# Kernel optimization log

Measured on AMD Instinct MI355X. Metric: run time of the kernel, lower is better.

## Reference

```python
import jax, jax.numpy as jnp
import numpy as np

N, L, D, W = 64, 514, 768, 256   # batch, padded token len (incl CLS/SEP), bert dim, max words
H1, H2 = 500, 300                # linear1 out, out_size
LN_EPS = 1e-5


def setup_inputs() -> dict:
    key = jax.random.key(0)
    ks = jax.random.split(key, 6)
    texts = jax.random.normal(ks[0], (N, L, D), dtype=jnp.float32)
    # contiguous ragged spans: lengths in {1,2}, cumulative ends <= 512 = L-2 always
    lens = jax.random.randint(ks[1], (N, W), 1, 3)
    word_ends = jnp.cumsum(lens, axis=1).astype(jnp.int32)
    word_starts = (word_ends - lens).astype(jnp.int32)
    word_length = jax.random.randint(ks[2], (N,), W // 2, W + 1).astype(jnp.int32)
    W1 = jax.random.normal(ks[3], (D, H1), dtype=jnp.float32) * np.float32(1.0 / np.sqrt(D))
    b1 = jnp.zeros((H1,), jnp.float32)
    W2 = jax.random.normal(ks[4], (H1, H2), dtype=jnp.float32) * np.float32(1.0 / np.sqrt(H1))
    b2 = jnp.zeros((H2,), jnp.float32)
    gamma = jnp.ones((H2,), jnp.float32)
    beta = jnp.zeros((H2,), jnp.float32)
    return dict(texts=texts, word_starts=word_starts, word_ends=word_ends,
                word_length=word_length, W1=W1, b1=b1, W2=W2, b2=b2,
                gamma=gamma, beta=beta)


def reference(texts, word_starts, word_ends, word_length, W1, b1, W2, b2, gamma, beta):
    # texts: (N, L, D) BERT output; drop [CLS]/[SEP]
    tok = texts[:, 1:-1, :]  # (N, L-2, D)
    # offset-based segment mean: prefix sums over token axis
    csum = jnp.concatenate([jnp.zeros_like(tok[:, :1]), jnp.cumsum(tok, axis=1)], axis=1)  # (N, L-1, D)
    e = word_ends[:, :, None].astype(jnp.int32)
    s = word_starts[:, :, None].astype(jnp.int32)
    seg_sum = jnp.take_along_axis(csum, e, axis=1) - jnp.take_along_axis(csum, s, axis=1)  # (N, W, D)
    cnt = (word_ends - word_starts).astype(texts.dtype)[:, :, None]
    pooled = seg_sum / jnp.maximum(cnt, 1.0)
    # pad_sequence semantics: words beyond word_length[i] are zero
    mask = (jnp.arange(W)[None, :] < word_length[:, None])[:, :, None]
    pooled = jnp.where(mask, pooled, jnp.zeros((), texts.dtype))
    # MLP + LayerNorm: norm(relu(linear2(relu(linear1(x)))))
    h = jax.nn.relu(pooled @ W1 + b1)
    h = jax.nn.relu(h @ W2 + b2)
    mu = jnp.mean(h, axis=-1, keepdims=True)
    var = jnp.mean(jnp.square(h - mu), axis=-1, keepdims=True)
    return (h - mu) * jax.lax.rsqrt(var + LN_EPS) * gamma + beta  # (N, W, 300)
```

## Files before the change

### kernel.cpp

```cpp
#include <hip/hip_runtime.h>
#include <hip/hip_bf16.h>


#define N_  64
#define L_  514
#define D_  768
#define W_  256
#define H1_ 500
#define H1P 512
#define H2_ 300
#define H2P 320
#define LN_EPS 1e-5f
#define M_  (N_ * W_)

typedef __bf16 bf16x8 __attribute__((ext_vector_type(8)));
typedef float  f32x4  __attribute__((ext_vector_type(4)));

__device__ __forceinline__ void load_lds16(const void* g, void* l) {
    __builtin_amdgcn_global_load_lds(
        (const __attribute__((address_space(1))) void*)g,
        (__attribute__((address_space(3))) void*)l, 16, 0, 0);
}

#define CONV1_ELEMS (H1P * D_)
#define CONV2_ELEMS (H2P * H1P)
#define CONV1_B ((CONV1_ELEMS + 191) / 192)
#define CONV2_B ((CONV2_ELEMS + 191) / 192)

__global__ __launch_bounds__(192) void prep_kernel(
    const float* __restrict__ texts, const int* __restrict__ wstart,
    const int* __restrict__ wend, const int* __restrict__ wlen,
    const float* __restrict__ W1, const float* __restrict__ W2,
    __hip_bfloat16* __restrict__ pooled, __hip_bfloat16* __restrict__ W1T,
    __hip_bfloat16* __restrict__ W2T)
{
    int b = blockIdx.x;
    if (b < M_) {
        int n = b >> 8;
        int w = b & (W_ - 1);
        int s = wstart[b], e = wend[b];
        bool live = (w < wlen[n]);
        int d = threadIdx.x * 4;
        float4 acc = make_float4(0.f, 0.f, 0.f, 0.f);
        if (live) {
            const float* base = texts + ((size_t)n * L_ + 1) * D_ + d;
            for (int i = s; i < e; ++i) {
                float4 v = *reinterpret_cast<const float4*>(base + (size_t)i * D_);
                acc.x += v.x; acc.y += v.y; acc.z += v.z; acc.w += v.w;
            }
            float inv = 1.0f / (float)max(e - s, 1);
            acc.x *= inv; acc.y *= inv; acc.z *= inv; acc.w *= inv;
        }
        union { __hip_bfloat16 h[4]; uint2 u; } o;
        o.h[0] = __float2bfloat16(acc.x); o.h[1] = __float2bfloat16(acc.y);
        o.h[2] = __float2bfloat16(acc.z); o.h[3] = __float2bfloat16(acc.w);
        *reinterpret_cast<uint2*>(pooled + (size_t)b * D_ + d) = o.u;
    } else if (b < M_ + CONV1_B) {
        int t = (b - M_) * 192 + threadIdx.x;
        if (t < CONV1_ELEMS) {
            int n = t / D_, k = t - n * D_;
            float v = (n < H1_) ? W1[(size_t)k * H1_ + n] : 0.f;
            W1T[t] = __float2bfloat16(v);
        }
    } else {
        int t = (b - M_ - CONV1_B) * 192 + threadIdx.x;
        if (t < CONV2_ELEMS) {
            int n = t >> 9, k = t & (H1P - 1);
            float v = (n < H2_ && k < H1_) ? W2[(size_t)k * H2_ + n] : 0.f;
            W2T[t] = __float2bfloat16(v);
        }
    }
}

__global__ __launch_bounds__(512, 1) void gemm1_kernel(
    const ushort* __restrict__ A, const ushort* __restrict__ B,
    const float* __restrict__ b1, ushort* __restrict__ h1)
{
    constexpr int BUFB = 24576;
    __shared__ __align__(16) char bufs[4 * BUFB];
    const int tid  = threadIdx.x;
    const int wave = tid >> 6, lane = tid & 63;
    const int wm = wave >> 1, wn = wave & 1;
    const int t256 = (blockIdx.x & 7) * 32 + (blockIdx.x >> 3);
    const int bm = (t256 >> 2) * 256, bn = (t256 & 3) * 128;
    const int lrow = lane >> 2, lslot = lane & 3;
    const int g = lane >> 4, fr = lane & 15;

    f32x4 acc[4][4] = {};

    auto stage = [&](int buf, int kt) {
        char* base = bufs + buf * BUFB;
        #pragma unroll
        for (int c0 = 0; c0 < 3; ++c0) {
            int c = wave + c0 * 8;
            int row; const ushort* src;
            if (c < 16) { row = c * 16 + lrow; src = A + (size_t)(bm + row) * D_; }
            else        { row = (c - 16) * 16 + lrow; src = B + (size_t)(bn + row) * D_; }
            int sslot = lslot ^ ((row >> 1) & 3);
            load_lds16(src + kt + sslot * 8, base + c * 1024);
        }
    };

    auto compute = [&](int t) {
        const char* base = bufs + (t & 3) * BUFB;
        bf16x8 af[4], bf[4];
        #pragma unroll
        for (int mi = 0; mi < 4; ++mi) {
            int r = wm * 64 + mi * 16 + fr;
            af[mi] = *(const bf16x8*)(base + r * 64 + ((g ^ ((r >> 1) & 3)) << 4));
        }
        #pragma unroll
        for (int ni = 0; ni < 4; ++ni) {
            int r = wn * 64 + ni * 16 + fr;
            bf[ni] = *(const bf16x8*)(base + 16384 + r * 64 + ((g ^ ((r >> 1) & 3)) << 4));
        }
        __builtin_amdgcn_s_setprio(1);
        #pragma unroll
        for (int mi = 0; mi < 4; ++mi)
            #pragma unroll
            for (int ni = 0; ni < 4; ++ni)
                acc[mi][ni] = __builtin_amdgcn_mfma_f32_16x16x32_bf16(
                    af[mi], bf[ni], acc[mi][ni], 0, 0, 0);
        __builtin_amdgcn_s_setprio(0);
    };

    stage(0, 0); stage(1, 32); stage(2, 64);
    for (int t = 0; t < 22; ++t) {
        asm volatile("s_waitcnt vmcnt(6)" ::: "memory");
        __builtin_amdgcn_s_barrier();
        if (t + 3 < 24) stage((t + 3) & 3, (t + 3) * 32);
        compute(t);
    }
    asm volatile("s_waitcnt vmcnt(3)" ::: "memory");
    __builtin_amdgcn_s_barrier();
    compute(22);
    asm volatile("s_waitcnt vmcnt(0)" ::: "memory");
    __builtin_amdgcn_s_barrier();
    compute(23);

    #pragma unroll
    for (int mi = 0; mi < 4; ++mi)
        #pragma unroll
        for (int ni = 0; ni < 4; ++ni) {
            int col = bn + wn * 64 + ni * 16 + fr;
            float bv = (col < H1_) ? b1[col] : 0.f;
            #pragma unroll
            for (int j = 0; j < 4; ++j) {
                int row = bm + wm * 64 + mi * 16 + g * 4 + j;
                float v = acc[mi][ni][j] + bv;
                ((__hip_bfloat16*)h1)[(size_t)row * H1P + col] =
                    __float2bfloat16(v > 0.f ? v : 0.f);
            }
        }
}

__global__ __launch_bounds__(512, 1) void gemm2_ln_kernel(
    const ushort* __restrict__ A, const ushort* __restrict__ B,
    const float* __restrict__ b2, const float* __restrict__ gamma,
    const float* __restrict__ beta, float* __restrict__ out)
{
    constexpr int BUFB = 24576;
    __shared__ __align__(16) char bufs[4 * BUFB];
    __shared__ float red[2][32][4][2];
    const int tid  = threadIdx.x;
    const int wave = tid >> 6, lane = tid & 63;
    const int wm = wave >> 2, wn = wave & 3;
    const int bm = blockIdx.x * 64;
    const int lrow = lane >> 2, lslot = lane & 3;
    const int g = lane >> 4, fr = lane & 15;

    f32x4 acc[2][5] = {};

    auto stage = [&](int buf, int kt) {
        char* base = bufs + buf * BUFB;
        #pragma unroll
        for (int c0 = 0; c0 < 3; ++c0) {
            int c = wave + c0 * 8;
            int row; const ushort* src;
            if (c < 4) { row = c * 16 + lrow; src = A + (size_t)(bm + row) * H1P; }
            else       { row = (c - 4) * 16 + lrow; src = B + (size_t)row * H1P; }
            int sslot = lslot ^ ((row >> 1) & 3);
            load_lds16(src + kt + sslot * 8, base + c * 1024);
        }
    };

    auto compute = [&](int t) {
        const char* base = bufs + (t & 3) * BUFB;
        bf16x8 af[2], bf[5];
        #pragma unroll
        for (int mi = 0; mi < 2; ++mi) {
            int r = wm * 32 + mi * 16 + fr;
            af[mi] = *(const bf16x8*)(base + r * 64 + ((g ^ ((r >> 1) & 3)) << 4));
        }
        #pragma unroll
        for (int ni = 0; ni < 5; ++ni) {
            int r = wn * 80 + ni * 16 + fr;
            bf[ni] = *(const bf16x8*)(base + 4096 + r * 64 + ((g ^ ((r >> 1) & 3)) << 4));
        }
        __builtin_amdgcn_s_setprio(1);
        #pragma unroll
        for (int mi = 0; mi < 2; ++mi)
            #pragma unroll
            for (int ni = 0; ni < 5; ++ni)
                acc[mi][ni] = __builtin_amdgcn_mfma_f32_16x16x32_bf16(
                    af[mi], bf[ni], acc[mi][ni], 0, 0, 0);
        __builtin_amdgcn_s_setprio(0);
    };

    stage(0, 0); stage(1, 32); stage(2, 64);
    for (int t = 0; t < 14; ++t) {
        asm volatile("s_waitcnt vmcnt(6)" ::: "memory");
        __builtin_amdgcn_s_barrier();
        if (t + 3 < 16) stage((t + 3) & 3, (t + 3) * 32);
        compute(t);
    }
    asm volatile("s_waitcnt vmcnt(3)" ::: "memory");
    __builtin_amdgcn_s_barrier();
    compute(14);
    asm volatile("s_waitcnt vmcnt(0)" ::: "memory");
    __builtin_amdgcn_s_barrier();
    compute(15);

    float vals[2][5][4];
    float rsum[2][4] = {}, rsq[2][4] = {};
    #pragma unroll
    for (int ni = 0; ni < 5; ++ni) {
        int col = wn * 80 + ni * 16 + fr;
        float bv = (col < H2_) ? b2[col] : 0.f;
        #pragma unroll
        for (int mi = 0; mi < 2; ++mi)
            #pragma unroll
            for (int j = 0; j < 4; ++j) {
                float v = acc[mi][ni][j] + bv;
                v = v > 0.f ? v : 0.f;
                vals[mi][ni][j] = v;
                rsum[mi][j] += v;
                rsq[mi][j]  += v * v;
            }
    }
    #pragma unroll
    for (int off = 1; off < 16; off <<= 1)
        #pragma unroll
        for (int mi = 0; mi < 2; ++mi)
            #pragma unroll
            for (int j = 0; j < 4; ++j) {
                rsum[mi][j] += __shfl_xor(rsum[mi][j], off);
                rsq[mi][j]  += __shfl_xor(rsq[mi][j], off);
            }
    if (fr == 0) {
        #pragma unroll
        for (int mi = 0; mi < 2; ++mi)
            #pragma unroll
            for (int j = 0; j < 4; ++j) {
                int r32 = mi * 16 + g * 4 + j;
                red[wm][r32][wn][0] = rsum[mi][j];
                red[wm][r32][wn][1] = rsq[mi][j];
            }
    }
    __syncthreads();
    #pragma unroll
    for (int mi = 0; mi < 2; ++mi) {
        #pragma unroll
        for (int j = 0; j < 4; ++j) {
            int r32 = mi * 16 + g * 4 + j;
            float S  = red[wm][r32][0][0] + red[wm][r32][1][0]
                     + red[wm][r32][2][0] + red[wm][r32][3][0];
            float SQ = red[wm][r32][0][1] + red[wm][r32][1][1]
                     + red[wm][r32][2][1] + red[wm][r32][3][1];
            float mu   = S * (1.0f / H2_);
            float var  = SQ * (1.0f / H2_) - mu * mu;
            float rstd = rsqrtf(var + LN_EPS);
            int row = bm + wm * 32 + r32;
            #pragma unroll
            for (int ni = 0; ni < 5; ++ni) {
                int col = wn * 80 + ni * 16 + fr;
                if (col < H2_)
                    out[(size_t)row * H2_ + col] =
                        (vals[mi][ni][j] - mu) * rstd * gamma[col] + beta[col];
            }
        }
    }
}

extern "C" void kernel_launch(void* const* d_in, const int* in_sizes, int n_in,
                              void* d_out, int out_size, void* d_ws, size_t ws_size,
                              hipStream_t stream)
{
    const float* texts  = (const float*)d_in[0];
    const int*   wstart = (const int*)  d_in[1];
    const int*   wend   = (const int*)  d_in[2];
    const int*   wlen   = (const int*)  d_in[3];
    const float* W1     = (const float*)d_in[4];
    const float* b1     = (const float*)d_in[5];
    const float* W2     = (const float*)d_in[6];
    const float* b2     = (const float*)d_in[7];
    const float* gamma  = (const float*)d_in[8];
    const float* beta   = (const float*)d_in[9];
    float* out = (float*)d_out;

    ushort* pooled = (ushort*)d_ws;
    ushort* h1     = pooled + (size_t)M_ * D_;
    ushort* W1T    = h1 + (size_t)M_ * H1P;
    ushort* W2T    = W1T + (size_t)H1P * D_;

    prep_kernel<<<M_ + CONV1_B + CONV2_B, 192, 0, stream>>>(
        texts, wstart, wend, wlen, W1, W2,
        (__hip_bfloat16*)pooled, (__hip_bfloat16*)W1T, (__hip_bfloat16*)W2T);

    gemm1_kernel<<<256, 512, 0, stream>>>(pooled, W1T, b1, h1);

    gemm2_ln_kernel<<<M_ / 64, 512, 0, stream>>>(h1, W2T, b2, gamma, beta, out);
}
```

Measured before the change: 57.10 us.

## Load GEMM B-operand fragments directly into registers, bypassing LDS staging

In both GEMM kernels, the weight (B) tiles are no longer staged through LDS. Each wave now loads its B fragments straight from global memory into registers, prefetched one k-step ahead with a double-buffered register pair. Only the A tile still goes through the LDS ring, which shrinks the LDS buffers and cuts LDS read/write traffic. The trade-offs are duplicated global/L2 reads of B across waves and more live VGPRs. The hand-tuned vmcnt waits now mix register and LDS loads, and in the tail iterations the pending count may no longer guarantee that the last A stage has landed before the barrier.

```diff
diff --git a/kernel.cpp b/kernel.cpp
--- a/kernel.cpp
+++ b/kernel.cpp
@@ -76,7 +76,7 @@
     const ushort* __restrict__ A, const ushort* __restrict__ B,
     const float* __restrict__ b1, ushort* __restrict__ h1)
 {
-    constexpr int BUFB = 24576;
+    constexpr int BUFB = 16384;
     __shared__ __align__(16) char bufs[4 * BUFB];
     const int tid  = threadIdx.x;
     const int wave = tid >> 6, lane = tid & 63;
@@ -88,55 +88,56 @@
 
     f32x4 acc[4][4] = {};
 
-    auto stage = [&](int buf, int kt) {
+    auto stageA = [&](int buf, int kt) {
         char* base = bufs + buf * BUFB;
         #pragma unroll
-        for (int c0 = 0; c0 < 3; ++c0) {
+        for (int c0 = 0; c0 < 2; ++c0) {
             int c = wave + c0 * 8;
-            int row; const ushort* src;
-            if (c < 16) { row = c * 16 + lrow; src = A + (size_t)(bm + row) * D_; }
-            else        { row = (c - 16) * 16 + lrow; src = B + (size_t)(bn + row) * D_; }
+            int row = c * 16 + lrow;
             int sslot = lslot ^ ((row >> 1) & 3);
-            load_lds16(src + kt + sslot * 8, base + c * 1024);
-        }
-    };
-
-    auto compute = [&](int t) {
+            load_lds16(A + (size_t)(bm + row) * D_ + kt + sslot * 8,
+                       base + c * 1024);
+        }
+    };
+    const ushort* Bw = B + (size_t)(bn + wn * 64 + fr) * D_ + g * 8;
+    auto loadB = [&](bf16x8* dst, int kt) {
+        #pragma unroll
+        for (int ni = 0; ni < 4; ++ni)
+            dst[ni] = *(const bf16x8*)(Bw + (size_t)(ni * 16) * D_ + kt);
+    };
+
+    auto compute = [&](int t, const bf16x8* bcur) {
         const char* base = bufs + (t & 3) * BUFB;
-        bf16x8 af[4], bf[4];
+        bf16x8 af[4];
         #pragma unroll
         for (int mi = 0; mi < 4; ++mi) {
             int r = wm * 64 + mi * 16 + fr;
             af[mi] = *(const bf16x8*)(base + r * 64 + ((g ^ ((r >> 1) & 3)) << 4));
         }
-        #pragma unroll
-        for (int ni = 0; ni < 4; ++ni) {
-            int r = wn * 64 + ni * 16 + fr;
-            bf[ni] = *(const bf16x8*)(base + 16384 + r * 64 + ((g ^ ((r >> 1) & 3)) << 4));
-        }
         __builtin_amdgcn_s_setprio(1);
         #pragma unroll
         for (int mi = 0; mi < 4; ++mi)
             #pragma unroll
             for (int ni = 0; ni < 4; ++ni)
                 acc[mi][ni] = __builtin_amdgcn_mfma_f32_16x16x32_bf16(
-                    af[mi], bf[ni], acc[mi][ni], 0, 0, 0);
+                    af[mi], bcur[ni], acc[mi][ni], 0, 0, 0);
         __builtin_amdgcn_s_setprio(0);
     };
 
-    stage(0, 0); stage(1, 32); stage(2, 64);
-    for (int t = 0; t < 22; ++t) {
-        asm volatile("s_waitcnt vmcnt(6)" ::: "memory");
+    bf16x8 bcur[4], bnext[4];
+    stageA(0, 0); stageA(1, 32); stageA(2, 64);
+    loadB(bcur, 0);
+
+    constexpr int NT = 24;
+    for (int t = 0; t < NT; ++t) {
+        asm volatile("s_waitcnt vmcnt(8)" ::: "memory");
         __builtin_amdgcn_s_barrier();
-        if (t + 3 < 24) stage((t + 3) & 3, (t + 3) * 32);
-        compute(t);
-    }
-    asm volatile("s_waitcnt vmcnt(3)" ::: "memory");
-    __builtin_amdgcn_s_barrier();
-    compute(22);
-    asm volatile("s_waitcnt vmcnt(0)" ::: "memory");
-    __builtin_amdgcn_s_barrier();
-    compute(23);
+        if (t + 1 < NT) loadB(bnext, (t + 1) * 32);
+        if (t + 3 < NT) stageA((t + 3) & 3, (t + 3) * 32);
+        compute(t, bcur);
+        #pragma unroll
+        for (int ni = 0; ni < 4; ++ni) bcur[ni] = bnext[ni];
+    }
 
     #pragma unroll
     for (int mi = 0; mi < 4; ++mi)
@@ -159,7 +160,7 @@
     const float* __restrict__ b2, const float* __restrict__ gamma,
     const float* __restrict__ beta, float* __restrict__ out)
 {
-    constexpr int BUFB = 24576;
+    constexpr int BUFB = 4096;
     __shared__ __align__(16) char bufs[4 * BUFB];
     __shared__ float red[2][32][4][2];
     const int tid  = threadIdx.x;
@@ -171,55 +172,53 @@
 
     f32x4 acc[2][5] = {};
 
-    auto stage = [&](int buf, int kt) {
-        char* base = bufs + buf * BUFB;
-        #pragma unroll
-        for (int c0 = 0; c0 < 3; ++c0) {
-            int c = wave + c0 * 8;
-            int row; const ushort* src;
-            if (c < 4) { row = c * 16 + lrow; src = A + (size_t)(bm + row) * H1P; }
-            else       { row = (c - 4) * 16 + lrow; src = B + (size_t)row * H1P; }
+    auto stageA = [&](int buf, int kt) {
+        if (wave < 4) {
+            int row = wave * 16 + lrow;
             int sslot = lslot ^ ((row >> 1) & 3);
-            load_lds16(src + kt + sslot * 8, base + c * 1024);
-        }
-    };
-
-    auto compute = [&](int t) {
+            load_lds16(A + (size_t)(bm + row) * H1P + kt + sslot * 8,
+                       bufs + buf * BUFB + wave * 1024);
+        }
+    };
+    const ushort* Bw = B + (size_t)(wn * 80 + fr) * H1P + g * 8;
+    auto loadB = [&](bf16x8* dst, int kt) {
+        #pragma unroll
+        for (int ni = 0; ni < 5; ++ni)
+            dst[ni] = *(const bf16x8*)(Bw + (size_t)(ni * 16) * H1P + kt);
+    };
+
+    auto compute = [&](int t, const bf16x8* bcur) {
         const char* base = bufs + (t & 3) * BUFB;
-        bf16x8 af[2], bf[5];
+        bf16x8 af[2];
         #pragma unroll
         for (int mi = 0; mi < 2; ++mi) {
             int r = wm * 32 + mi * 16 + fr;
             af[mi] = *(const bf16x8*)(base + r * 64 + ((g ^ ((r >> 1) & 3)) << 4));
         }
-        #pragma unroll
-        for (int ni = 0; ni < 5; ++ni) {
-            int r = wn * 80 + ni * 16 + fr;
-            bf[ni] = *(const bf16x8*)(base + 4096 + r * 64 + ((g ^ ((r >> 1) & 3)) << 4));
-        }
         __builtin_amdgcn_s_setprio(1);
         #pragma unroll
         for (int mi = 0; mi < 2; ++mi)
             #pragma unroll
             for (int ni = 0; ni < 5; ++ni)
                 acc[mi][ni] = __builtin_amdgcn_mfma_f32_16x16x32_bf16(
-                    af[mi], bf[ni], acc[mi][ni], 0, 0, 0);
+                    af[mi], bcur[ni], acc[mi][ni], 0, 0, 0);
         __builtin_amdgcn_s_setprio(0);
     };
 
-    stage(0, 0); stage(1, 32); stage(2, 64);
-    for (int t = 0; t < 14; ++t) {
-        asm volatile("s_waitcnt vmcnt(6)" ::: "memory");
+    bf16x8 bcur[5], bnext[5];
+    stageA(0, 0); stageA(1, 32); stageA(2, 64);
+    loadB(bcur, 0);
+
+    constexpr int NT = 16;
+    for (int t = 0; t < NT; ++t) {
+        asm volatile("s_waitcnt vmcnt(7)" ::: "memory");
         __builtin_amdgcn_s_barrier();
-        if (t + 3 < 16) stage((t + 3) & 3, (t + 3) * 32);
-        compute(t);
-    }
-    asm volatile("s_waitcnt vmcnt(3)" ::: "memory");
-    __builtin_amdgcn_s_barrier();
-    compute(14);
-    asm volatile("s_waitcnt vmcnt(0)" ::: "memory");
-    __builtin_amdgcn_s_barrier();
-    compute(15);
+        if (t + 1 < NT) loadB(bnext, (t + 1) * 32);
+        if (t + 3 < NT) stageA((t + 3) & 3, (t + 3) * 32);
+        compute(t, bcur);
+        #pragma unroll
+        for (int ni = 0; ni < 5; ++ni) bcur[ni] = bnext[ni];
+    }
 
     float vals[2][5][4];
     float rsum[2][4] = {}, rsq[2][4] = {};
```

New measurement: 90.33 us. 58.2% more time.

## Fuse segment-mean pooling into GEMM1 A-tile loads, drop pooled buffer

Applied to the files above, without the earlier changes.

Segment-mean pooling moves out of the prep kernel and into GEMM1's A operand staging. Each thread loads fp32 token rows for its word, averages them, converts to bf16 and writes the result into swizzled LDS. This removes the pooled bf16 intermediate's write and re-read, leaving only a small weight-conversion kernel. In exchange the pipeline drops from a 4-stage async global-to-LDS prefetch to a 2-stage register-prefetch loop with full barriers. Each of the 4 column blocks per row block now re-reads the fp32 texts rows, so more raw bytes are fetched and latency hiding may be weaker.

```diff
diff --git a/kernel.cpp b/kernel.cpp
--- a/kernel.cpp
+++ b/kernel.cpp
@@ -24,95 +24,109 @@
 
 #define CONV1_ELEMS (H1P * D_)
 #define CONV2_ELEMS (H2P * H1P)
-#define CONV1_B ((CONV1_ELEMS + 191) / 192)
-#define CONV2_B ((CONV2_ELEMS + 191) / 192)
-
-__global__ __launch_bounds__(192) void prep_kernel(
+#define CONV1_B (CONV1_ELEMS / 256)
+#define CONV2_B (CONV2_ELEMS / 256)
+
+__global__ __launch_bounds__(256) void conv_kernel(
+    const float* __restrict__ W1, const float* __restrict__ W2,
+    __hip_bfloat16* __restrict__ W1T, __hip_bfloat16* __restrict__ W2T)
+{
+    int b = blockIdx.x;
+    if (b < CONV1_B) {
+        int t = b * 256 + threadIdx.x;
+        int n = t / D_, k = t - n * D_;
+        float v = (n < H1_) ? W1[(size_t)k * H1_ + n] : 0.f;
+        W1T[t] = __float2bfloat16(v);
+    } else {
+        int t = (b - CONV1_B) * 256 + threadIdx.x;
+        int n = t >> 9, k = t & (H1P - 1);
+        float v = (n < H2_ && k < H1_) ? W2[(size_t)k * H2_ + n] : 0.f;
+        W2T[t] = __float2bfloat16(v);
+    }
+}
+
+__global__ __launch_bounds__(512, 1) void gemm1_kernel(
     const float* __restrict__ texts, const int* __restrict__ wstart,
     const int* __restrict__ wend, const int* __restrict__ wlen,
-    const float* __restrict__ W1, const float* __restrict__ W2,
-    __hip_bfloat16* __restrict__ pooled, __hip_bfloat16* __restrict__ W1T,
-    __hip_bfloat16* __restrict__ W2T)
+    const ushort* __restrict__ B, const float* __restrict__ b1,
+    ushort* __restrict__ h1)
 {
-    int b = blockIdx.x;
-    if (b < M_) {
-        int n = b >> 8;
-        int w = b & (W_ - 1);
-        int s = wstart[b], e = wend[b];
-        bool live = (w < wlen[n]);
-        int d = threadIdx.x * 4;
-        float4 acc = make_float4(0.f, 0.f, 0.f, 0.f);
-        if (live) {
-            const float* base = texts + ((size_t)n * L_ + 1) * D_ + d;
-            for (int i = s; i < e; ++i) {
-                float4 v = *reinterpret_cast<const float4*>(base + (size_t)i * D_);
-                acc.x += v.x; acc.y += v.y; acc.z += v.z; acc.w += v.w;
-            }
-            float inv = 1.0f / (float)max(e - s, 1);
-            acc.x *= inv; acc.y *= inv; acc.z *= inv; acc.w *= inv;
-        }
-        union { __hip_bfloat16 h[4]; uint2 u; } o;
-        o.h[0] = __float2bfloat16(acc.x); o.h[1] = __float2bfloat16(acc.y);
-        o.h[2] = __float2bfloat16(acc.z); o.h[3] = __float2bfloat16(acc.w);
-        *reinterpret_cast<uint2*>(pooled + (size_t)b * D_ + d) = o.u;
-    } else if (b < M_ + CONV1_B) {
-        int t = (b - M_) * 192 + threadIdx.x;
-        if (t < CONV1_ELEMS) {
-            int n = t / D_, k = t - n * D_;
-            float v = (n < H1_) ? W1[(size_t)k * H1_ + n] : 0.f;
-            W1T[t] = __float2bfloat16(v);
-        }
-    } else {
-        int t = (b - M_ - CONV1_B) * 192 + threadIdx.x;
-        if (t < CONV2_ELEMS) {
-            int n = t >> 9, k = t & (H1P - 1);
-            float v = (n < H2_ && k < H1_) ? W2[(size_t)k * H2_ + n] : 0.f;
-            W2T[t] = __float2bfloat16(v);
-        }
-    }
-}
-
-__global__ __launch_bounds__(512, 1) void gemm1_kernel(
-    const ushort* __restrict__ A, const ushort* __restrict__ B,
-    const float* __restrict__ b1, ushort* __restrict__ h1)
-{
-    constexpr int BUFB = 24576;
-    __shared__ __align__(16) char bufs[4 * BUFB];
+    __shared__ __align__(16) char Abuf[2][16384];
+    __shared__ __align__(16) char Bbuf[2][8192];
+
     const int tid  = threadIdx.x;
     const int wave = tid >> 6, lane = tid & 63;
     const int wm = wave >> 1, wn = wave & 1;
     const int t256 = (blockIdx.x & 7) * 32 + (blockIdx.x >> 3);
-    const int bm = (t256 >> 2) * 256, bn = (t256 & 3) * 128;
+    const int n  = t256 >> 2;
+    const int bm = n * 256, bn = (t256 & 3) * 128;
     const int lrow = lane >> 2, lslot = lane & 3;
     const int g = lane >> 4, fr = lane & 15;
 
+    const int prow  = tid >> 1;
+    const int phalf = tid & 1;
+    const int s = wstart[bm + prow];
+    const int e = wend[bm + prow];
+    const bool live = (prow < wlen[n]);
+    const bool two  = live && (e - s > 1);
+    const float inv = live ? 1.0f / (float)max(e - s, 1) : 0.f;
+    const float* trow = texts + ((size_t)n * L_ + 1 + s) * D_ + phalf * 16;
+
     f32x4 acc[4][4] = {};
 
-    auto stage = [&](int buf, int kt) {
-        char* base = bufs + buf * BUFB;
-        #pragma unroll
-        for (int c0 = 0; c0 < 3; ++c0) {
-            int c = wave + c0 * 8;
-            int row; const ushort* src;
-            if (c < 16) { row = c * 16 + lrow; src = A + (size_t)(bm + row) * D_; }
-            else        { row = (c - 16) * 16 + lrow; src = B + (size_t)(bn + row) * D_; }
-            int sslot = lslot ^ ((row >> 1) & 3);
-            load_lds16(src + kt + sslot * 8, base + c * 1024);
-        }
-    };
-
+    auto issueA = [&](float4* pf, int kt) {
+        if (live) {
+            const float4* p0 = (const float4*)(trow + kt);
+            pf[0] = p0[0]; pf[1] = p0[1]; pf[2] = p0[2]; pf[3] = p0[3];
+        }
+        if (two) {
+            const float4* p1 = (const float4*)(trow + kt + D_);
+            pf[4] = p1[0]; pf[5] = p1[1]; pf[6] = p1[2]; pf[7] = p1[3];
+        }
+    };
+    auto writeA = [&](const float4* pf, int buf) {
+        union { __hip_bfloat16 h[8]; uint4 u; } o0, o1;
+        #pragma unroll
+        for (int j = 0; j < 4; ++j) {
+            float4 a = pf[j], b2v = pf[4 + j];
+            float x0 = two ? a.x + b2v.x : a.x;
+            float x1 = two ? a.y + b2v.y : a.y;
+            float x2 = two ? a.z + b2v.z : a.z;
+            float x3 = two ? a.w + b2v.w : a.w;
+            x0 = live ? x0 * inv : 0.f;  x1 = live ? x1 * inv : 0.f;
+            x2 = live ? x2 * inv : 0.f;  x3 = live ? x3 * inv : 0.f;
+            if (j < 2) {
+                o0.h[j*4+0] = __float2bfloat16(x0); o0.h[j*4+1] = __float2bfloat16(x1);
+                o0.h[j*4+2] = __float2bfloat16(x2); o0.h[j*4+3] = __float2bfloat16(x3);
+            } else {
+                o1.h[(j-2)*4+0] = __float2bfloat16(x0); o1.h[(j-2)*4+1] = __float2bfloat16(x1);
+                o1.h[(j-2)*4+2] = __float2bfloat16(x2); o1.h[(j-2)*4+3] = __float2bfloat16(x3);
+            }
+        }
+        const int swz = (prow >> 1) & 3;
+        char* base = Abuf[buf] + prow * 64;
+        *(uint4*)(base + (((phalf*2 + 0) ^ swz) << 4)) = o0.u;
+        *(uint4*)(base + (((phalf*2 + 1) ^ swz) << 4)) = o1.u;
+    };
+    auto stageB = [&](int buf, int kt) {
+        int row = wave * 16 + lrow;
+        int sslot = lslot ^ ((row >> 1) & 3);
+        load_lds16(B + (size_t)(bn + row) * D_ + kt + sslot * 8,
+                   Bbuf[buf] + wave * 1024);
+    };
     auto compute = [&](int t) {
-        const char* base = bufs + (t & 3) * BUFB;
+        const char* ab = Abuf[t & 1];
+        const char* bb = Bbuf[t & 1];
         bf16x8 af[4], bf[4];
         #pragma unroll
         for (int mi = 0; mi < 4; ++mi) {
             int r = wm * 64 + mi * 16 + fr;
-            af[mi] = *(const bf16x8*)(base + r * 64 + ((g ^ ((r >> 1) & 3)) << 4));
+            af[mi] = *(const bf16x8*)(ab + r * 64 + ((g ^ ((r >> 1) & 3)) << 4));
         }
         #pragma unroll
         for (int ni = 0; ni < 4; ++ni) {
             int r = wn * 64 + ni * 16 + fr;
-            bf[ni] = *(const bf16x8*)(base + 16384 + r * 64 + ((g ^ ((r >> 1) & 3)) << 4));
+            bf[ni] = *(const bf16x8*)(bb + r * 64 + ((g ^ ((r >> 1) & 3)) << 4));
         }
         __builtin_amdgcn_s_setprio(1);
         #pragma unroll
@@ -124,19 +138,22 @@
         __builtin_amdgcn_s_setprio(0);
     };
 
-    stage(0, 0); stage(1, 32); stage(2, 64);
-    for (int t = 0; t < 22; ++t) {
-        asm volatile("s_waitcnt vmcnt(6)" ::: "memory");
-        __builtin_amdgcn_s_barrier();
-        if (t + 3 < 24) stage((t + 3) & 3, (t + 3) * 32);
+    float4 pf[8];
+    issueA(pf, 0);
+    stageB(0, 0);
+    writeA(pf, 0);
+    __syncthreads();
+
+    constexpr int NT = 24;
+    for (int t = 0; t < NT; ++t) {
+        if (t + 1 < NT) {
+            issueA(pf, (t + 1) * 32);
+            stageB((t + 1) & 1, (t + 1) * 32);
+        }
         compute(t);
-    }
-    asm volatile("s_waitcnt vmcnt(3)" ::: "memory");
-    __builtin_amdgcn_s_barrier();
-    compute(22);
-    asm volatile("s_waitcnt vmcnt(0)" ::: "memory");
-    __builtin_amdgcn_s_barrier();
-    compute(23);
+        if (t + 1 < NT) writeA(pf, (t + 1) & 1);
+        __syncthreads();
+    }
 
     #pragma unroll
     for (int mi = 0; mi < 4; ++mi)
@@ -298,16 +315,15 @@
     const float* beta   = (const float*)d_in[9];
     float* out = (float*)d_out;
 
-    ushort* pooled = (ushort*)d_ws;
-    ushort* h1     = pooled + (size_t)M_ * D_;
-    ushort* W1T    = h1 + (size_t)M_ * H1P;
-    ushort* W2T    = W1T + (size_t)H1P * D_;
-
-    prep_kernel<<<M_ + CONV1_B + CONV2_B, 192, 0, stream>>>(
-        texts, wstart, wend, wlen, W1, W2,
-        (__hip_bfloat16*)pooled, (__hip_bfloat16*)W1T, (__hip_bfloat16*)W2T);
-
-    gemm1_kernel<<<256, 512, 0, stream>>>(pooled, W1T, b1, h1);
+    ushort* h1  = (ushort*)d_ws;
+    ushort* W1T = h1 + (size_t)M_ * H1P;
+    ushort* W2T = W1T + (size_t)H1P * D_;
+
+    conv_kernel<<<CONV1_B + CONV2_B, 256, 0, stream>>>(
+        W1, W2, (__hip_bfloat16*)W1T, (__hip_bfloat16*)W2T);
+
+    gemm1_kernel<<<256, 512, 0, stream>>>(
+        texts, wstart, wend, wlen, W1T, b1, h1);
 
     gemm2_ln_kernel<<<M_ / 64, 512, 0, stream>>>(h1, W2T, b2, gamma, beta, out);
 }
```

Result: slower. 71.56 us (+25.3%).

## Fuse prep, GEMM1 and GEMM2+LayerNorm into one cooperative persistent kernel

Applied to the files above, without the earlier changes.

Replaces the three launches (pooling plus weight transposes, GEMM1, GEMM2 with LayerNorm) with a single cooperative kernel of 256 blocks, using grid-wide syncs between the phases. Pooling is redone per block so that each wave handles 8 words with 3 float4 loads per lane. The goal is to remove launch gaps and per-kernel ramp-up and tail time. In exchange the kernel pays for grid.sync, and the pooling phase now runs on only 256 blocks instead of about 16K small blocks, which may reduce memory-level parallelism for the pooling reads.

```diff
diff --git a/kernel.cpp b/kernel.cpp
--- a/kernel.cpp
+++ b/kernel.cpp
@@ -1,6 +1,9 @@
 #include <hip/hip_runtime.h>
 #include <hip/hip_bf16.h>
-
+#include <hip/hip_cooperative_groups.h>
+
+
+namespace cg = cooperative_groups;
 
 #define N_  64
 #define L_  514
@@ -12,6 +15,8 @@
 #define H2P 320
 #define LN_EPS 1e-5f
 #define M_  (N_ * W_)
+#define CONV1_ELEMS (H1P * D_)
+#define CONV2_ELEMS (H2P * H1P)
 
 typedef __bf16 bf16x8 __attribute__((ext_vector_type(8)));
 typedef float  f32x4  __attribute__((ext_vector_type(4)));
@@ -22,261 +27,252 @@
         (__attribute__((address_space(3))) void*)l, 16, 0, 0);
 }
 
-#define CONV1_ELEMS (H1P * D_)
-#define CONV2_ELEMS (H2P * H1P)
-#define CONV1_B ((CONV1_ELEMS + 191) / 192)
-#define CONV2_B ((CONV2_ELEMS + 191) / 192)
-
-__global__ __launch_bounds__(192) void prep_kernel(
+__device__ __forceinline__ uint2 pack4(f32x4 v) {
+    union { __hip_bfloat16 h[4]; uint2 u; } o;
+    o.h[0] = __float2bfloat16(v[0]); o.h[1] = __float2bfloat16(v[1]);
+    o.h[2] = __float2bfloat16(v[2]); o.h[3] = __float2bfloat16(v[3]);
+    return o.u;
+}
+
+__global__ __launch_bounds__(512, 1) void fused_kernel(
     const float* __restrict__ texts, const int* __restrict__ wstart,
     const int* __restrict__ wend, const int* __restrict__ wlen,
     const float* __restrict__ W1, const float* __restrict__ W2,
-    __hip_bfloat16* __restrict__ pooled, __hip_bfloat16* __restrict__ W1T,
-    __hip_bfloat16* __restrict__ W2T)
+    const float* __restrict__ b1, const float* __restrict__ b2,
+    const float* __restrict__ gamma, const float* __restrict__ beta,
+    ushort* __restrict__ pooled, ushort* __restrict__ h1,
+    ushort* __restrict__ W1T, ushort* __restrict__ W2T,
+    float* __restrict__ out)
 {
-    int b = blockIdx.x;
-    if (b < M_) {
-        int n = b >> 8;
-        int w = b & (W_ - 1);
-        int s = wstart[b], e = wend[b];
-        bool live = (w < wlen[n]);
-        int d = threadIdx.x * 4;
-        float4 acc = make_float4(0.f, 0.f, 0.f, 0.f);
-        if (live) {
-            const float* base = texts + ((size_t)n * L_ + 1) * D_ + d;
-            for (int i = s; i < e; ++i) {
-                float4 v = *reinterpret_cast<const float4*>(base + (size_t)i * D_);
-                acc.x += v.x; acc.y += v.y; acc.z += v.z; acc.w += v.w;
-            }
-            float inv = 1.0f / (float)max(e - s, 1);
-            acc.x *= inv; acc.y *= inv; acc.z *= inv; acc.w *= inv;
-        }
-        union { __hip_bfloat16 h[4]; uint2 u; } o;
-        o.h[0] = __float2bfloat16(acc.x); o.h[1] = __float2bfloat16(acc.y);
-        o.h[2] = __float2bfloat16(acc.z); o.h[3] = __float2bfloat16(acc.w);
-        *reinterpret_cast<uint2*>(pooled + (size_t)b * D_ + d) = o.u;
-    } else if (b < M_ + CONV1_B) {
-        int t = (b - M_) * 192 + threadIdx.x;
-        if (t < CONV1_ELEMS) {
-            int n = t / D_, k = t - n * D_;
-            float v = (n < H1_) ? W1[(size_t)k * H1_ + n] : 0.f;
-            W1T[t] = __float2bfloat16(v);
-        }
-    } else {
-        int t = (b - M_ - CONV1_B) * 192 + threadIdx.x;
-        if (t < CONV2_ELEMS) {
-            int n = t >> 9, k = t & (H1P - 1);
-            float v = (n < H2_ && k < H1_) ? W2[(size_t)k * H2_ + n] : 0.f;
-            W2T[t] = __float2bfloat16(v);
-        }
-    }
-}
-
-__global__ __launch_bounds__(512, 1) void gemm1_kernel(
-    const ushort* __restrict__ A, const ushort* __restrict__ B,
-    const float* __restrict__ b1, ushort* __restrict__ h1)
-{
-    constexpr int BUFB = 24576;
-    __shared__ __align__(16) char bufs[4 * BUFB];
-    const int tid  = threadIdx.x;
+    __shared__ __align__(16) char bufs[4 * 24576];
+    __shared__ float red[2][32][4][2];
+
+    const int b = blockIdx.x;
+    const int tid = threadIdx.x;
     const int wave = tid >> 6, lane = tid & 63;
-    const int wm = wave >> 1, wn = wave & 1;
-    const int t256 = (blockIdx.x & 7) * 32 + (blockIdx.x >> 3);
-    const int bm = (t256 >> 2) * 256, bn = (t256 & 3) * 128;
+    const int swz = (b & 7) * 32 + (b >> 3);
     const int lrow = lane >> 2, lslot = lane & 3;
     const int g = lane >> 4, fr = lane & 15;
 
-    f32x4 acc[4][4] = {};
-
-    auto stage = [&](int buf, int kt) {
-        char* base = bufs + buf * BUFB;
-        #pragma unroll
-        for (int c0 = 0; c0 < 3; ++c0) {
-            int c = wave + c0 * 8;
-            int row; const ushort* src;
-            if (c < 16) { row = c * 16 + lrow; src = A + (size_t)(bm + row) * D_; }
-            else        { row = (c - 16) * 16 + lrow; src = B + (size_t)(bn + row) * D_; }
-            int sslot = lslot ^ ((row >> 1) & 3);
-            load_lds16(src + kt + sslot * 8, base + c * 1024);
-        }
-    };
-
-    auto compute = [&](int t) {
-        const char* base = bufs + (t & 3) * BUFB;
-        bf16x8 af[4], bf[4];
-        #pragma unroll
-        for (int mi = 0; mi < 4; ++mi) {
-            int r = wm * 64 + mi * 16 + fr;
-            af[mi] = *(const bf16x8*)(base + r * 64 + ((g ^ ((r >> 1) & 3)) << 4));
-        }
-        #pragma unroll
-        for (int ni = 0; ni < 4; ++ni) {
-            int r = wn * 64 + ni * 16 + fr;
-            bf[ni] = *(const bf16x8*)(base + 16384 + r * 64 + ((g ^ ((r >> 1) & 3)) << 4));
-        }
-        __builtin_amdgcn_s_setprio(1);
+    {
+        for (int t = b * 512 + tid; t < CONV1_ELEMS; t += 256 * 512) {
+            int nn = t / D_, k = t - nn * D_;
+            float v = (nn < H1_) ? W1[(size_t)k * H1_ + nn] : 0.f;
+            ((__hip_bfloat16*)W1T)[t] = __float2bfloat16(v);
+        }
+        for (int t = b * 512 + tid; t < CONV2_ELEMS; t += 256 * 512) {
+            int nn = t >> 9, k = t & (H1P - 1);
+            float v = (nn < H2_ && k < H1_) ? W2[(size_t)k * H2_ + nn] : 0.f;
+            ((__hip_bfloat16*)W2T)[t] = __float2bfloat16(v);
+        }
+        const int n = swz >> 2, q = swz & 3;
+        for (int i = 0; i < 8; ++i) {
+            int wl  = q * 64 + wave * 8 + i;
+            int idx = n * W_ + wl;
+            int s = wstart[idx], e = wend[idx];
+            bool live = wl < wlen[n];
+            float inv = 1.0f / (float)max(e - s, 1);
+            f32x4 a0 = {}, a1 = {}, a2 = {};
+            if (live) {
+                const float* base = texts + ((size_t)n * L_ + 1 + s) * D_ + lane * 4;
+                for (int r = 0; r < e - s; ++r) {
+                    const float* p = base + (size_t)r * D_;
+                    a0 += *(const f32x4*)(p);
+                    a1 += *(const f32x4*)(p + 256);
+                    a2 += *(const f32x4*)(p + 512);
+                }
+                a0 *= inv; a1 *= inv; a2 *= inv;
+            }
+            __hip_bfloat16* dst = (__hip_bfloat16*)pooled + (size_t)idx * D_ + lane * 4;
+            *(uint2*)(dst)       = pack4(a0);
+            *(uint2*)(dst + 256) = pack4(a1);
+            *(uint2*)(dst + 512) = pack4(a2);
+        }
+    }
+    cg::this_grid().sync();
+
+    {
+        const int wm = wave >> 1, wn = wave & 1;
+        const int bm = (swz >> 2) * 256, bn = (swz & 3) * 128;
+        f32x4 acc[4][4] = {};
+
+        auto stage = [&](int buf, int kt) {
+            char* base = bufs + buf * 24576;
+            #pragma unroll
+            for (int c0 = 0; c0 < 3; ++c0) {
+                int c = wave + c0 * 8;
+                int row; const ushort* src;
+                if (c < 16) { row = c * 16 + lrow;        src = pooled + (size_t)(bm + row) * D_; }
+                else        { row = (c - 16) * 16 + lrow; src = W1T + (size_t)(bn + row) * D_; }
+                int sslot = lslot ^ ((row >> 1) & 3);
+                load_lds16(src + kt + sslot * 8, base + c * 1024);
+            }
+        };
+        auto compute = [&](int t) {
+            const char* base = bufs + (t & 3) * 24576;
+            bf16x8 af[4], bf[4];
+            #pragma unroll
+            for (int mi = 0; mi < 4; ++mi) {
+                int r = wm * 64 + mi * 16 + fr;
+                af[mi] = *(const bf16x8*)(base + r * 64 + ((g ^ ((r >> 1) & 3)) << 4));
+            }
+            #pragma unroll
+            for (int ni = 0; ni < 4; ++ni) {
+                int r = wn * 64 + ni * 16 + fr;
+                bf[ni] = *(const bf16x8*)(base + 16384 + r * 64 + ((g ^ ((r >> 1) & 3)) << 4));
+            }
+            __builtin_amdgcn_s_setprio(1);
+            #pragma unroll
+            for (int mi = 0; mi < 4; ++mi)
+                #pragma unroll
+                for (int ni = 0; ni < 4; ++ni)
+                    acc[mi][ni] = __builtin_amdgcn_mfma_f32_16x16x32_bf16(
+                        af[mi], bf[ni], acc[mi][ni], 0, 0, 0);
+            __builtin_amdgcn_s_setprio(0);
+        };
+
+        stage(0, 0); stage(1, 32); stage(2, 64);
+        for (int t = 0; t < 22; ++t) {
+            asm volatile("s_waitcnt vmcnt(6)" ::: "memory");
+            __builtin_amdgcn_s_barrier();
+            if (t + 3 < 24) stage((t + 3) & 3, (t + 3) * 32);
+            compute(t);
+        }
+        asm volatile("s_waitcnt vmcnt(3)" ::: "memory");
+        __builtin_amdgcn_s_barrier();
+        compute(22);
+        asm volatile("s_waitcnt vmcnt(0)" ::: "memory");
+        __builtin_amdgcn_s_barrier();
+        compute(23);
+
         #pragma unroll
         for (int mi = 0; mi < 4; ++mi)
             #pragma unroll
-            for (int ni = 0; ni < 4; ++ni)
-                acc[mi][ni] = __builtin_amdgcn_mfma_f32_16x16x32_bf16(
-                    af[mi], bf[ni], acc[mi][ni], 0, 0, 0);
-        __builtin_amdgcn_s_setprio(0);
-    };
-
-    stage(0, 0); stage(1, 32); stage(2, 64);
-    for (int t = 0; t < 22; ++t) {
-        asm volatile("s_waitcnt vmcnt(6)" ::: "memory");
+            for (int ni = 0; ni < 4; ++ni) {
+                int col = bn + wn * 64 + ni * 16 + fr;
+                float bv = (col < H1_) ? b1[col] : 0.f;
+                #pragma unroll
+                for (int j = 0; j < 4; ++j) {
+                    int row = bm + wm * 64 + mi * 16 + g * 4 + j;
+                    float v = acc[mi][ni][j] + bv;
+                    ((__hip_bfloat16*)h1)[(size_t)row * H1P + col] =
+                        __float2bfloat16(v > 0.f ? v : 0.f);
+                }
+            }
+    }
+    cg::this_grid().sync();
+
+    {
+        const int wm = wave >> 2, wn = wave & 3;
+        const int bm = swz * 64;
+        f32x4 acc[2][5] = {};
+
+        auto stage = [&](int buf, int kt) {
+            char* base = bufs + buf * 24576;
+            #pragma unroll
+            for (int c0 = 0; c0 < 3; ++c0) {
+                int c = wave + c0 * 8;
+                int row; const ushort* src;
+                if (c < 4) { row = c * 16 + lrow;       src = h1 + (size_t)(bm + row) * H1P; }
+                else       { row = (c - 4) * 16 + lrow; src = W2T + (size_t)row * H1P; }
+                int sslot = lslot ^ ((row >> 1) & 3);
+                load_lds16(src + kt + sslot * 8, base + c * 1024);
+            }
+        };
+        auto compute = [&](int t) {
+            const char* base = bufs + (t & 3) * 24576;
+            bf16x8 af[2], bf[5];
+            #pragma unroll
+            for (int mi = 0; mi < 2; ++mi) {
+                int r = wm * 32 + mi * 16 + fr;
+                af[mi] = *(const bf16x8*)(base + r * 64 + ((g ^ ((r >> 1) & 3)) << 4));
+            }
+            #pragma unroll
+            for (int ni = 0; ni < 5; ++ni) {
+                int r = wn * 80 + ni * 16 + fr;
+                bf[ni] = *(const bf16x8*)(base + 4096 + r * 64 + ((g ^ ((r >> 1) & 3)) << 4));
+            }
+            __builtin_amdgcn_s_setprio(1);
+            #pragma unroll
+            for (int mi = 0; mi < 2; ++mi)
+                #pragma unroll
+                for (int ni = 0; ni < 5; ++ni)
+                    acc[mi][ni] = __builtin_amdgcn_mfma_f32_16x16x32_bf16(
+                        af[mi], bf[ni], acc[mi][ni], 0, 0, 0);
+            __builtin_amdgcn_s_setprio(0);
+        };
+
+        stage(0, 0); stage(1, 32); stage(2, 64);
+        for (int t = 0; t < 14; ++t) {
+            asm volatile("s_waitcnt vmcnt(6)" ::: "memory");
+            __builtin_amdgcn_s_barrier();
+            if (t + 3 < 16) stage((t + 3) & 3, (t + 3) * 32);
+            compute(t);
+        }
+        asm volatile("s_waitcnt vmcnt(3)" ::: "memory");
         __builtin_amdgcn_s_barrier();
-        if (t + 3 < 24) stage((t + 3) & 3, (t + 3) * 32);
-        compute(t);
-    }
-    asm volatile("s_waitcnt vmcnt(3)" ::: "memory");
-    __builtin_amdgcn_s_barrier();
-    compute(22);
-    asm volatile("s_waitcnt vmcnt(0)" ::: "memory");
-    __builtin_amdgcn_s_barrier();
-    compute(23);
-
-    #pragma unroll
-    for (int mi = 0; mi < 4; ++mi)
+        compute(14);
+        asm volatile("s_waitcnt vmcnt(0)" ::: "memory");
+        __builtin_amdgcn_s_barrier();
+        compute(15);
+
+        float vals[2][5][4];
+        float rsum[2][4] = {}, rsq[2][4] = {};
         #pragma unroll
-        for (int ni = 0; ni < 4; ++ni) {
-            int col = bn + wn * 64 + ni * 16 + fr;
-            float bv = (col < H1_) ? b1[col] : 0.f;
-            #pragma unroll
-            for (int j = 0; j < 4; ++j) {
-                int row = bm + wm * 64 + mi * 16 + g * 4 + j;
-                float v = acc[mi][ni][j] + bv;
-                ((__hip_bfloat16*)h1)[(size_t)row * H1P + col] =
-                    __float2bfloat16(v > 0.f ? v : 0.f);
-            }
-        }
-}
-
-__global__ __launch_bounds__(512, 1) void gemm2_ln_kernel(
-    const ushort* __restrict__ A, const ushort* __restrict__ B,
-    const float* __restrict__ b2, const float* __restrict__ gamma,
-    const float* __restrict__ beta, float* __restrict__ out)
-{
-    constexpr int BUFB = 24576;
-    __shared__ __align__(16) char bufs[4 * BUFB];
-    __shared__ float red[2][32][4][2];
-    const int tid  = threadIdx.x;
-    const int wave = tid >> 6, lane = tid & 63;
-    const int wm = wave >> 2, wn = wave & 3;
-    const int bm = blockIdx.x * 64;
-    const int lrow = lane >> 2, lslot = lane & 3;
-    const int g = lane >> 4, fr = lane & 15;
-
-    f32x4 acc[2][5] = {};
-
-    auto stage = [&](int buf, int kt) {
-        char* base = bufs + buf * BUFB;
+        for (int ni = 0; ni < 5; ++ni) {
+            int col = wn * 80 + ni * 16 + fr;
+            float bv = (col < H2_) ? b2[col] : 0.f;
+            #pragma unroll
+            for (int mi = 0; mi < 2; ++mi)
+                #pragma unroll
+                for (int j = 0; j < 4; ++j) {
+                    float v = acc[mi][ni][j] + bv;
+                    v = v > 0.f ? v : 0.f;
+                    vals[mi][ni][j] = v;
+                    rsum[mi][j] += v;
+                    rsq[mi][j]  += v * v;
+                }
+        }
         #pragma unroll
-        for (int c0 = 0; c0 < 3; ++c0) {
-            int c = wave + c0 * 8;
-            int row; const ushort* src;
-            if (c < 4) { row = c * 16 + lrow; src = A + (size_t)(bm + row) * H1P; }
-            else       { row = (c - 4) * 16 + lrow; src = B + (size_t)row * H1P; }
-            int sslot = lslot ^ ((row >> 1) & 3);
-            load_lds16(src + kt + sslot * 8, base + c * 1024);
-        }
-    };
-
-    auto compute = [&](int t) {
-        const char* base = bufs + (t & 3) * BUFB;
-        bf16x8 af[2], bf[5];
+        for (int off = 1; off < 16; off <<= 1)
+            #pragma unroll
+            for (int mi = 0; mi < 2; ++mi)
+                #pragma unroll
+                for (int j = 0; j < 4; ++j) {
+                    rsum[mi][j] += __shfl_xor(rsum[mi][j], off);
+                    rsq[mi][j]  += __shfl_xor(rsq[mi][j], off);
+                }
+        if (fr == 0) {
+            #pragma unroll
+            for (int mi = 0; mi < 2; ++mi)
+                #pragma unroll
+                for (int j = 0; j < 4; ++j) {
+                    int r32 = mi * 16 + g * 4 + j;
+                    red[wm][r32][wn][0] = rsum[mi][j];
+                    red[wm][r32][wn][1] = rsq[mi][j];
+                }
+        }
+        __syncthreads();
         #pragma unroll
         for (int mi = 0; mi < 2; ++mi) {
-            int r = wm * 32 + mi * 16 + fr;
-            af[mi] = *(const bf16x8*)(base + r * 64 + ((g ^ ((r >> 1) & 3)) << 4));
-        }
-        #pragma unroll
-        for (int ni = 0; ni < 5; ++ni) {
-            int r = wn * 80 + ni * 16 + fr;
-            bf[ni] = *(const bf16x8*)(base + 4096 + r * 64 + ((g ^ ((r >> 1) & 3)) << 4));
-        }
-        __builtin_amdgcn_s_setprio(1);
-        #pragma unroll
-        for (int mi = 0; mi < 2; ++mi)
-            #pragma unroll
-            for (int ni = 0; ni < 5; ++ni)
-                acc[mi][ni] = __builtin_amdgcn_mfma_f32_16x16x32_bf16(
-                    af[mi], bf[ni], acc[mi][ni], 0, 0, 0);
-        __builtin_amdgcn_s_setprio(0);
-    };
-
-    stage(0, 0); stage(1, 32); stage(2, 64);
-    for (int t = 0; t < 14; ++t) {
-        asm volatile("s_waitcnt vmcnt(6)" ::: "memory");
-        __builtin_amdgcn_s_barrier();
-        if (t + 3 < 16) stage((t + 3) & 3, (t + 3) * 32);
-        compute(t);
-    }
-    asm volatile("s_waitcnt vmcnt(3)" ::: "memory");
-    __builtin_amdgcn_s_barrier();
-    compute(14);
-    asm volatile("s_waitcnt vmcnt(0)" ::: "memory");
-    __builtin_amdgcn_s_barrier();
-    compute(15);
-
-    float vals[2][5][4];
-    float rsum[2][4] = {}, rsq[2][4] = {};
-    #pragma unroll
-    for (int ni = 0; ni < 5; ++ni) {
-        int col = wn * 80 + ni * 16 + fr;
-        float bv = (col < H2_) ? b2[col] : 0.f;
-        #pragma unroll
-        for (int mi = 0; mi < 2; ++mi)
-            #pragma unroll
-            for (int j = 0; j < 4; ++j) {
-                float v = acc[mi][ni][j] + bv;
-                v = v > 0.f ? v : 0.f;
-                vals[mi][ni][j] = v;
-                rsum[mi][j] += v;
-                rsq[mi][j]  += v * v;
-            }
-    }
-    #pragma unroll
-    for (int off = 1; off < 16; off <<= 1)
-        #pragma unroll
-        for (int mi = 0; mi < 2; ++mi)
-            #pragma unroll
-            for (int j = 0; j < 4; ++j) {
-                rsum[mi][j] += __shfl_xor(rsum[mi][j], off);
-                rsq[mi][j]  += __shfl_xor(rsq[mi][j], off);
-            }
-    if (fr == 0) {
-        #pragma unroll
-        for (int mi = 0; mi < 2; ++mi)
             #pragma unroll
             for (int j = 0; j < 4; ++j) {
                 int r32 = mi * 16 + g * 4 + j;
-                red[wm][r32][wn][0] = rsum[mi][j];
-                red[wm][r32][wn][1] = rsq[mi][j];
-            }
-    }
-    __syncthreads();
-    #pragma unroll
-    for (int mi = 0; mi < 2; ++mi) {
-        #pragma unroll
-        for (int j = 0; j < 4; ++j) {
-            int r32 = mi * 16 + g * 4 + j;
-            float S  = red[wm][r32][0][0] + red[wm][r32][1][0]
-                     + red[wm][r32][2][0] + red[wm][r32][3][0];
-            float SQ = red[wm][r32][0][1] + red[wm][r32][1][1]
-                     + red[wm][r32][2][1] + red[wm][r32][3][1];
-            float mu   = S * (1.0f / H2_);
-            float var  = SQ * (1.0f / H2_) - mu * mu;
-            float rstd = rsqrtf(var + LN_EPS);
-            int row = bm + wm * 32 + r32;
-            #pragma unroll
-            for (int ni = 0; ni < 5; ++ni) {
-                int col = wn * 80 + ni * 16 + fr;
-                if (col < H2_)
-                    out[(size_t)row * H2_ + col] =
-                        (vals[mi][ni][j] - mu) * rstd * gamma[col] + beta[col];
+                float S  = red[wm][r32][0][0] + red[wm][r32][1][0]
+                         + red[wm][r32][2][0] + red[wm][r32][3][0];
+                float SQ = red[wm][r32][0][1] + red[wm][r32][1][1]
+                         + red[wm][r32][2][1] + red[wm][r32][3][1];
+                float mu   = S * (1.0f / H2_);
+                float var  = SQ * (1.0f / H2_) - mu * mu;
+                float rstd = rsqrtf(var + LN_EPS);
+                int row = bm + wm * 32 + r32;
+                #pragma unroll
+                for (int ni = 0; ni < 5; ++ni) {
+                    int col = wn * 80 + ni * 16 + fr;
+                    if (col < H2_)
+                        out[(size_t)row * H2_ + col] =
+                            (vals[mi][ni][j] - mu) * rstd * gamma[col] + beta[col];
+                }
             }
         }
     }
@@ -303,11 +299,11 @@
     ushort* W1T    = h1 + (size_t)M_ * H1P;
     ushort* W2T    = W1T + (size_t)H1P * D_;
 
-    prep_kernel<<<M_ + CONV1_B + CONV2_B, 192, 0, stream>>>(
-        texts, wstart, wend, wlen, W1, W2,
-        (__hip_bfloat16*)pooled, (__hip_bfloat16*)W1T, (__hip_bfloat16*)W2T);
-
-    gemm1_kernel<<<256, 512, 0, stream>>>(pooled, W1T, b1, h1);
-
-    gemm2_ln_kernel<<<M_ / 64, 512, 0, stream>>>(h1, W2T, b2, gamma, beta, out);
+    void* args[] = { (void*)&texts, (void*)&wstart, (void*)&wend, (void*)&wlen,
+                     (void*)&W1, (void*)&W2, (void*)&b1, (void*)&b2,
+                     (void*)&gamma, (void*)&beta,
+                     (void*)&pooled, (void*)&h1, (void*)&W1T, (void*)&W2T,
+                     (void*)&out };
+    hipLaunchCooperativeKernel((void*)fused_kernel, dim3(256), dim3(512),
+                               args, 0, stream);
 }
```

Measured after the change: 140.2 us. +145.5%, slower.
